# Performance work log

Measured on AMD Instinct MI355X. Metric: run time of the kernel, lower is better.

The kernel has to match this reference:

```python
import jax, jax.numpy as jnp
import numpy as np

KS = 3          # deformable kernel size
N = KS * KS     # 9 sampling points
PAD = 1         # zero padding before sampling


def setup_inputs() -> dict:
    key = jax.random.key(0)
    k = jax.random.split(key, 4)
    b, c, h, w = 8, 64, 128, 128
    x = jax.random.normal(k[0], (b, c, h, w), jnp.float32)
    # offset-prediction conv: Conv2d(c, 2*N, 3, padding=1, stride=1) with bias
    w_off = jax.random.normal(k[1], (2 * N, c, 3, 3), jnp.float32) * 0.01
    b_off = jax.random.normal(k[2], (2 * N,), jnp.float32) * 0.01
    # main conv: Conv2d(c, c, 3, stride=3, bias=None) applied to rearranged samples
    w_conv = jax.random.normal(k[3], (c, c, KS, KS), jnp.float32) * (1.0 / np.sqrt(c * N))
    return {"x": x, "w_off": w_off, "b_off": b_off, "w_conv": w_conv}


def _deform_conv2d(x, w_off, b_off, w_conv):
    b, c, h, w = x.shape
    # 1) predict offsets: (b, 2N, h, w)
    offset = jax.lax.conv_general_dilated(
        x, w_off, (1, 1), ((PAD, PAD), (PAD, PAD)),
        dimension_numbers=("NCHW", "OIHW", "NCHW"))
    offset = offset + b_off[None, :, None, None]
    offset = offset.transpose(0, 2, 3, 1)  # (b, h, w, 2N), first N = rows, last N = cols

    # 2) sampling positions p = p_0 + p_n + offset (in zero-padded coords)
    dx, dy = jnp.meshgrid(
        jnp.arange(-(KS - 1) // 2, (KS - 1) // 2 + 1),
        jnp.arange(-(KS - 1) // 2, (KS - 1) // 2 + 1), indexing="ij")
    pn_x = dx.reshape(-1).astype(x.dtype)  # (N,)
    pn_y = dy.reshape(-1).astype(x.dtype)
    r0 = jnp.arange(1, h + 1, dtype=x.dtype)  # p_0 starts at 1 (padding shift)
    c0 = jnp.arange(1, w + 1, dtype=x.dtype)
    p_x = offset[..., :N] + pn_x + r0[None, :, None, None]   # (b,h,w,N)
    p_y = offset[..., N:] + pn_y + c0[None, None, :, None]

    xp = jnp.pad(x, ((0, 0), (0, 0), (PAD, PAD), (PAD, PAD)))
    Hp, Wp = h + 2 * PAD, w + 2 * PAD

    fx = jnp.floor(p_x)
    fy = jnp.floor(p_y)
    q_lt_x = jnp.clip(fx, 0, Hp - 1).astype(jnp.int32)
    q_lt_y = jnp.clip(fy, 0, Wp - 1).astype(jnp.int32)
    q_rb_x = jnp.clip(fx + 1, 0, Hp - 1).astype(jnp.int32)
    q_rb_y = jnp.clip(fy + 1, 0, Wp - 1).astype(jnp.int32)
    p_x = jnp.clip(p_x, 0, Hp - 1)
    p_y = jnp.clip(p_y, 0, Wp - 1)

    # bilinear weights (b,h,w,N); q values are non-differentiable (int)
    g_lt = (1 + (q_lt_x - p_x)) * (1 + (q_lt_y - p_y))
    g_rb = (1 - (q_rb_x - p_x)) * (1 - (q_rb_y - p_y))
    g_lb = (1 + (q_lt_x - p_x)) * (1 - (q_rb_y - p_y))
    g_rt = (1 - (q_rb_x - p_x)) * (1 + (q_lt_y - p_y))

    xp_flat = xp.reshape(b, c, Hp * Wp)

    def gather(qx, qy):
        idx = (qx * Wp + qy).reshape(b, 1, h * w * N)
        out = jnp.take_along_axis(
            xp_flat, jnp.broadcast_to(idx, (b, c, h * w * N)), axis=2)
        return out.reshape(b, c, h, w, N)

    x_off = (g_lt[:, None] * gather(q_lt_x, q_lt_y)
             + g_rb[:, None] * gather(q_rb_x, q_rb_y)
             + g_lb[:, None] * gather(q_lt_x, q_rb_y)
             + g_rt[:, None] * gather(q_rb_x, q_lt_y))  # (b,c,h,w,N)

    # 3) final KSxKS conv with stride KS over the rearranged samples is exactly
    #    a contraction over the N sampling points (sample n = kernel tap (i,j), n=i*KS+j)
    out = jnp.einsum("bchwn,ocn->bohw", x_off, w_conv.reshape(c, c, N))
    return out


def reference(x, w_off, b_off, w_conv):
    return _deform_conv2d(x, w_off, b_off, w_conv) + x
```

## Files before the change

### kernel.cpp

```cpp
#include <hip/hip_runtime.h>


typedef _Float16 h2    __attribute__((ext_vector_type(2)));
typedef _Float16 f16x8 __attribute__((ext_vector_type(8)));
typedef float    f32x4 __attribute__((ext_vector_type(4)));

#define MFMAH(a, b, c) __builtin_amdgcn_mfma_f32_16x16x32_f16(a, b, c, 0, 0, 0)
#define GTAG 0x40000000
#define OFFS 21

__device__ __forceinline__ h2 bch2(unsigned u) { return __builtin_bit_cast(h2, u); }
__device__ __forceinline__ unsigned bcu(h2 v) { return __builtin_bit_cast(unsigned, v); }
__device__ __forceinline__ unsigned short f2h(float f) {
    return __builtin_bit_cast(unsigned short, (_Float16)f);
}

__global__ __launch_bounds__(256) void k_prep_xt(const float* __restrict__ x,
                                                 unsigned short* __restrict__ xt) {
    __shared__ float xs[64][129];
    const int bh = blockIdx.x;
    const int h = bh & 127, b = bh >> 7;
    const float* xr = x + ((size_t)b * 64 * 128 + h) * 128;
    for (int idx = threadIdx.x; idx < 8192; idx += 256) {
        int c = idx >> 7, w = idx & 127;
        xs[c][w] = xr[(size_t)c * 16384 + w];
    }
    __syncthreads();
    unsigned short* xto = xt + ((size_t)bh << 13);
    for (int j = threadIdx.x; j < 1024; j += 256) {
        int w = j >> 3, c0 = (j & 7) << 3;
        unsigned short tmp[8];
#pragma unroll
        for (int e = 0; e < 8; ++e) tmp[e] = f2h(xs[c0 + e][w]);
        *(uint4*)(xto + w * 64 + c0) = *(const uint4*)tmp;
    }
}

__global__ void k_prep_w(const float* __restrict__ w_conv, const float* __restrict__ w_off,
                         unsigned short* __restrict__ w_m2, unsigned short* __restrict__ woff2) {
    int t = blockIdx.x * 256 + threadIdx.x;
    if (t < 36864) {
        int r = t & 511;
        int fid = t >> 9;
        int l15 = r >> 5, q4 = (r >> 3) & 3, e = t & 7;
        int chunk = fid & 1, of = (fid >> 1) & 3, n = fid >> 3;
        int o = of * 16 + l15, c = chunk * 32 + q4 * 8 + e;
        w_m2[t] = f2h(w_conv[(o * 64 + c) * 9 + n]);
    }
    int t2 = t - 36864;
    if (t2 >= 0 && t2 < 18432) {
        int r = t2 & 511;
        int fid = t2 >> 9;
        int l15 = r >> 5, q4 = (r >> 3) & 3, e = t2 & 7;
        int kc = fid & 1, half = (fid >> 1) & 1, rj = fid >> 2;
        int k = half * 16 + l15, c = kc * 32 + q4 * 8 + e;
        woff2[t2] = (k < 18) ? f2h(w_off[(k * 64 + c) * 9 + rj]) : (unsigned short)0;
    }
}

__global__ __launch_bounds__(256, 2) void k_fused(
    const float* __restrict__ x, const unsigned short* __restrict__ xt,
    const unsigned short* __restrict__ w_m2, const unsigned short* __restrict__ woff2,
    const float* __restrict__ b_off, float* __restrict__ out) {

    __shared__ __align__(16) unsigned char raw[420 * 128];
    __shared__ int   atab[9][64][4];
    __shared__ uint4 gtab[9][64];
    __shared__ float offv[64 * OFFS];
    __shared__ int   sfb;

    const int wk = ((blockIdx.x & 7) << 8) + (blockIdx.x >> 3);
    const int b = wk >> 8, h = (wk >> 1) & 127, wt = (wk & 1) << 6;

    const int tid  = threadIdx.x;
    const int lane = tid & 63, wid = tid >> 6;
    const int l15  = lane & 15, q4 = lane >> 4;
    const int lofs = ((l15 << 2) + q4) << 3;
    const int px   = wid * 16 + l15;

    const unsigned short* xtb = xt + ((size_t)b << 20);

    if (tid == 0) sfb = 0;

    for (int idx = tid; idx < 3360; idx += 256) {
        int rec = idx >> 3, cc = idx & 7;
        int row = rec / 70, col = rec - row * 70;
        int xr = h - 2 + row, xc = wt - 3 + col;
        uint4 v = make_uint4(0, 0, 0, 0);
        if (xr >= 0 && xr < 128 && xc >= 0 && xc < 128)
            v = *(const uint4*)(xtb + ((((size_t)xr << 7) + xc) << 6) + (cc << 3));
        *(uint4*)(raw + (rec << 7) + ((cc ^ (col & 7)) << 4)) = v;
    }
    __syncthreads();

    {
        f32x4 o0 = {0.f, 0.f, 0.f, 0.f}, o1 = {0.f, 0.f, 0.f, 0.f};
#pragma unroll
        for (int rj = 0; rj < 9; ++rj) {
            const int dr = rj / 3, dj = rj % 3;
            const int colw = px + dj + 2;
            const int recb = (dr + 1) * 70 + colw;
            const int swz  = colw & 7;
#pragma unroll
            for (int kc = 0; kc < 2; ++kc) {
                f16x8 bfrag = *(const f16x8*)(raw + (recb << 7) + ((((kc << 2) + q4) ^ swz) << 4));
                f16x8 a0 = *(const f16x8*)((const _Float16*)woff2 + ((((rj * 2 + 0) << 1) + kc) << 9) + lofs);
                f16x8 a1 = *(const f16x8*)((const _Float16*)woff2 + ((((rj * 2 + 1) << 1) + kc) << 9) + lofs);
                o0 = MFMAH(a0, bfrag, o0);
                o1 = MFMAH(a1, bfrag, o1);
            }
        }
#pragma unroll
        for (int rg = 0; rg < 4; ++rg) {
            int o = q4 * 4 + rg;
            offv[px * OFFS + o] = o0[rg] + b_off[o];
            int o1i = 16 + o;
            if (o1i < 18) offv[px * OFFS + o1i] = o1[rg] + b_off[o1i];
        }
    }
    __syncthreads();

    for (int idx = tid; idx < 576; idx += 256) {
        const int n = idx >> 6, p = idx & 63;
        float ox = offv[p * OFFS + n], oy = offv[p * OFFS + 9 + n];
        float pxf = ox + (float)(n / 3 - 1) + (float)(h + 1);
        float pyf = oy + (float)(n % 3 - 1) + (float)(wt + p + 1);
        float fx = floorf(pxf), fy = floorf(pyf);
        float fxc  = fminf(fmaxf(fx, 0.f), 129.f);
        float fyc  = fminf(fmaxf(fy, 0.f), 129.f);
        float fxc1 = fminf(fmaxf(fx + 1.f, 0.f), 129.f);
        float fyc1 = fminf(fmaxf(fy + 1.f, 0.f), 129.f);
        int qltx = (int)fxc, qlty = (int)fyc, qrbx = (int)fxc1, qrby = (int)fyc1;
        pxf = fminf(fmaxf(pxf, 0.f), 129.f);
        pyf = fminf(fmaxf(pyf, 0.f), 129.f);
        float glt = (1.f + (fxc  - pxf)) * (1.f + (fyc  - pyf));
        float grb = (1.f - (fxc1 - pxf)) * (1.f - (fyc1 - pyf));
        float glb = (1.f + (fxc  - pxf)) * (1.f - (fyc1 - pyf));
        float grt = (1.f - (fxc1 - pxf)) * (1.f + (fyc  - pyf));
        bool vlx = (qltx >= 1) & (qltx <= 128), vly = (qlty >= 1) & (qlty <= 128);
        bool vrx = (qrbx >= 1) & (qrbx <= 128), vry = (qrby >= 1) & (qrby <= 128);

        auto enc = [&](int qx, int qy, bool val) -> int {
            if (!val) return 0;
            int wr = qx - h + 1;
            int wc = qy - wt + 2;
            if (wr >= 0 && wr < 6 && wc >= 0 && wc < 70)
                return ((wr * 70 + wc) << 7) | ((wc & 7) << 4);
            return GTAG | ((((qx - 1) << 7) + (qy - 1)) << 6);
        };
        int a0 = enc(qltx, qlty, vlx & vly);
        int a1 = enc(qrbx, qrby, vrx & vry);
        int a2 = enc(qltx, qrby, vlx & vry);
        int a3 = enc(qrbx, qlty, vrx & vly);
        if ((a0 | a1 | a2 | a3) & GTAG) sfb = 1;
        if (!(vlx & vly)) glt = 0.f;
        if (!(vrx & vry)) grb = 0.f;
        if (!(vlx & vry)) glb = 0.f;
        if (!(vrx & vly)) grt = 0.f;
        auto pk = [](float g) -> unsigned {
            _Float16 t = (_Float16)g;
            h2 r = {t, t};
            return __builtin_bit_cast(unsigned, r);
        };
        *(int4*)&atab[n][p][0] = make_int4(a0, a1, a2, a3);
        gtab[n][p] = make_uint4(pk(glt), pk(grb), pk(glb), pk(grt));
    }
    __syncthreads();

    const size_t obase = ((size_t)b * 64 * 128 + h) * 128 + wt + px;
    float xres[4][4];
#pragma unroll
    for (int of = 0; of < 4; ++of)
#pragma unroll
        for (int rg = 0; rg < 4; ++rg)
            xres[of][rg] = x[obase + (size_t)(of * 16 + q4 * 4 + rg) * 16384];

    f32x4 acc[4];
#pragma unroll
    for (int of = 0; of < 4; ++of) acc[of] = (f32x4){0.f, 0.f, 0.f, 0.f};

    const _Float16* wmh = (const _Float16*)w_m2;
    f16x8 wreg[2][2][4];
#pragma unroll
    for (int of = 0; of < 4; ++of) {
        wreg[0][0][of] = *(const f16x8*)(wmh + (((of << 1) + 0) << 9) + lofs);
        wreg[0][1][of] = *(const f16x8*)(wmh + (((of << 1) + 1) << 9) + lofs);
    }

    auto blend = [&](const uint4* clo, const uint4* chi, uint4 gq, f16x8& bfr0, f16x8& bfr1) {
        h2 g0 = bch2(gq.x), g1 = bch2(gq.y), g2 = bch2(gq.z), g3 = bch2(gq.w);
        const unsigned* c0 = (const unsigned*)&clo[0];
        const unsigned* c1 = (const unsigned*)&clo[1];
        const unsigned* c2 = (const unsigned*)&clo[2];
        const unsigned* c3 = (const unsigned*)&clo[3];
        const unsigned* e0 = (const unsigned*)&chi[0];
        const unsigned* e1 = (const unsigned*)&chi[1];
        const unsigned* e2 = (const unsigned*)&chi[2];
        const unsigned* e3 = (const unsigned*)&chi[3];
        unsigned owl[4], owh[4];
#pragma unroll
        for (int d = 0; d < 4; ++d) {
            h2 sl = bch2(c0[d]) * g0;
            sl = __builtin_elementwise_fma(bch2(c1[d]), g1, sl);
            sl = __builtin_elementwise_fma(bch2(c2[d]), g2, sl);
            sl = __builtin_elementwise_fma(bch2(c3[d]), g3, sl);
            owl[d] = bcu(sl);
            h2 sh = bch2(e0[d]) * g0;
            sh = __builtin_elementwise_fma(bch2(e1[d]), g1, sh);
            sh = __builtin_elementwise_fma(bch2(e2[d]), g2, sh);
            sh = __builtin_elementwise_fma(bch2(e3[d]), g3, sh);
            owh[d] = bcu(sh);
        }
        bfr0 = __builtin_bit_cast(f16x8, *(const uint4*)owl);
        bfr1 = __builtin_bit_cast(f16x8, *(const uint4*)owh);
    };

    if (!sfb) {
#pragma unroll
        for (int n = 0; n < 9; ++n) {
            if (n < 8) {
                const _Float16* wn1 = wmh + ((n + 1) << 12);
#pragma unroll
                for (int of = 0; of < 4; ++of) {
                    wreg[(n + 1) & 1][0][of] = *(const f16x8*)(wn1 + (((of << 1) + 0) << 9) + lofs);
                    wreg[(n + 1) & 1][1][of] = *(const f16x8*)(wn1 + (((of << 1) + 1) << 9) + lofs);
                }
            }
            const int4  av = *(const int4*)&atab[n][px][0];
            const uint4 gq = gtab[n][px];
            const int ee[4] = {av.x, av.y, av.z, av.w};
            uint4 clo[4], chi[4];
#pragma unroll
            for (int j = 0; j < 4; ++j) {
                const unsigned char* lp = raw + (ee[j] & ~127);
                int sl = ((q4 ^ (ee[j] >> 4)) & 7) << 4;
                clo[j] = *(const uint4*)(lp + sl);
                chi[j] = *(const uint4*)(lp + (sl ^ 64));
            }
            f16x8 bfr0, bfr1;
            blend(clo, chi, gq, bfr0, bfr1);
#pragma unroll
            for (int of = 0; of < 4; ++of) {
                acc[of] = MFMAH(wreg[n & 1][0][of], bfr0, acc[of]);
                acc[of] = MFMAH(wreg[n & 1][1][of], bfr1, acc[of]);
            }
        }
    } else {
        for (int n = 0; n < 9; ++n) {
            const int4  av = *(const int4*)&atab[n][px][0];
            const uint4 gq = gtab[n][px];
            const int ee[4] = {av.x, av.y, av.z, av.w};
            uint4 clo[4], chi[4];
#pragma unroll
            for (int j = 0; j < 4; ++j) {
                int e = ee[j];
                if (e & GTAG) {
                    const unsigned short* gp = xtb + (e & (GTAG - 1));
                    clo[j] = *(const uint4*)(gp + (q4 << 3));
                    chi[j] = *(const uint4*)(gp + (q4 << 3) + 32);
                } else {
                    const unsigned char* lp = raw + (e & ~127);
                    int sl = ((q4 ^ (e >> 4)) & 7) << 4;
                    clo[j] = *(const uint4*)(lp + sl);
                    chi[j] = *(const uint4*)(lp + (sl ^ 64));
                }
            }
            f16x8 bfr0, bfr1;
            blend(clo, chi, gq, bfr0, bfr1);
            const _Float16* wn = wmh + (n << 12);
#pragma unroll
            for (int of = 0; of < 4; ++of) {
                f16x8 a0 = *(const f16x8*)(wn + (((of << 1) + 0) << 9) + lofs);
                f16x8 a1 = *(const f16x8*)(wn + (((of << 1) + 1) << 9) + lofs);
                acc[of] = MFMAH(a0, bfr0, acc[of]);
                acc[of] = MFMAH(a1, bfr1, acc[of]);
            }
        }
    }

#pragma unroll
    for (int of = 0; of < 4; ++of)
#pragma unroll
        for (int rg = 0; rg < 4; ++rg)
            out[obase + (size_t)(of * 16 + q4 * 4 + rg) * 16384] = acc[of][rg] + xres[of][rg];
}

extern "C" void kernel_launch(void* const* d_in, const int* in_sizes, int n_in,
                              void* d_out, int out_size, void* d_ws, size_t ws_size,
                              hipStream_t stream) {
    const float* x      = (const float*)d_in[0];
    const float* w_off  = (const float*)d_in[1];
    const float* b_off  = (const float*)d_in[2];
    const float* w_conv = (const float*)d_in[3];

    unsigned short* xt    = (unsigned short*)d_ws;
    unsigned short* w_m2  = xt + (size_t)8 * 128 * 128 * 64;
    unsigned short* woff2 = w_m2 + 9 * 64 * 64;

    hipLaunchKernelGGL(k_prep_xt, dim3(1024), dim3(256), 0, stream, x, xt);
    hipLaunchKernelGGL(k_prep_w,  dim3(216),  dim3(256), 0, stream, w_conv, w_off, w_m2, woff2);
    hipLaunchKernelGGL(k_fused,   dim3(2048), dim3(256), 0, stream,
                       x, xt, w_m2, woff2, b_off, (float*)d_out);
}
```

Baseline: 93.24 us.

## Shrink LDS with rolling 4-row ring buffer and inline bilinear setup per tap

The fused kernel now keeps a 4-row ring buffer of the input window in LDS instead of 6 rows, streaming rows 4 and 5 in while taps are processed, with extra barriers. It drops the per-tap address and weight tables and stores offsets as fp16. Bilinear indices and weights are recomputed inline in each tap, and launch bounds are raised to 4 blocks per CU. The goal is higher occupancy from the smaller LDS footprint, at the cost of more ALU work per tap, fp16 offset precision, and the slow path now reading every corner from global memory.

```diff
diff --git a/kernel.cpp b/kernel.cpp
--- a/kernel.cpp
+++ b/kernel.cpp
@@ -6,13 +6,17 @@
 typedef float    f32x4 __attribute__((ext_vector_type(4)));
 
 #define MFMAH(a, b, c) __builtin_amdgcn_mfma_f32_16x16x32_f16(a, b, c, 0, 0, 0)
-#define GTAG 0x40000000
-#define OFFS 21
-
-__device__ __forceinline__ h2 bch2(unsigned u) { return __builtin_bit_cast(h2, u); }
-__device__ __forceinline__ unsigned bcu(h2 v) { return __builtin_bit_cast(unsigned, v); }
+
 __device__ __forceinline__ unsigned short f2h(float f) {
     return __builtin_bit_cast(unsigned short, (_Float16)f);
+}
+__device__ __forceinline__ float h2f_bits(unsigned u) {
+    return (float)__builtin_bit_cast(_Float16, (unsigned short)(u & 0xffffu));
+}
+__device__ __forceinline__ unsigned dup16(float g) {
+    _Float16 t = (_Float16)g;
+    h2 r = {t, t};
+    return __builtin_bit_cast(unsigned, r);
 }
 
 __global__ __launch_bounds__(256) void k_prep_xt(const float* __restrict__ x,
@@ -58,16 +62,14 @@
     }
 }
 
-__global__ __launch_bounds__(256, 2) void k_fused(
+__global__ __launch_bounds__(256, 4) void k_fused(
     const float* __restrict__ x, const unsigned short* __restrict__ xt,
     const unsigned short* __restrict__ w_m2, const unsigned short* __restrict__ woff2,
     const float* __restrict__ b_off, float* __restrict__ out) {
 
-    __shared__ __align__(16) unsigned char raw[420 * 128];
-    __shared__ int   atab[9][64][4];
-    __shared__ uint4 gtab[9][64];
-    __shared__ float offv[64 * OFFS];
-    __shared__ int   sfb;
+    __shared__ __align__(16) unsigned char raw[4 * 70 * 128];
+    __shared__ __align__(16) _Float16 offv[64 * 24];
+    __shared__ int sfb;
 
     const int wk = ((blockIdx.x & 7) << 8) + (blockIdx.x >> 3);
     const int b = wk >> 8, h = (wk >> 1) & 127, wt = (wk & 1) << 6;
@@ -79,13 +81,14 @@
     const int px   = wid * 16 + l15;
 
     const unsigned short* xtb = xt + ((size_t)b << 20);
+    const _Float16* wmh  = (const _Float16*)w_m2;
 
     if (tid == 0) sfb = 0;
 
-    for (int idx = tid; idx < 3360; idx += 256) {
+    for (int idx = tid; idx < 2240; idx += 256) {
         int rec = idx >> 3, cc = idx & 7;
-        int row = rec / 70, col = rec - row * 70;
-        int xr = h - 2 + row, xc = wt - 3 + col;
+        int rl = rec / 70, col = rec - rl * 70;
+        int xr = h - 2 + rl, xc = wt - 3 + col;
         uint4 v = make_uint4(0, 0, 0, 0);
         if (xr >= 0 && xr < 128 && xc >= 0 && xc < 128)
             v = *(const uint4*)(xtb + ((((size_t)xr << 7) + xc) << 6) + (cc << 3));
@@ -110,85 +113,44 @@
                 o1 = MFMAH(a1, bfrag, o1);
             }
         }
+        float4 bo = *(const float4*)(b_off + (q4 << 2));
+        float2 bo2 = *(const float2*)(b_off + 16);
+        const float bov[4] = {bo.x, bo.y, bo.z, bo.w};
 #pragma unroll
         for (int rg = 0; rg < 4; ++rg) {
-            int o = q4 * 4 + rg;
-            offv[px * OFFS + o] = o0[rg] + b_off[o];
-            int o1i = 16 + o;
-            if (o1i < 18) offv[px * OFFS + o1i] = o1[rg] + b_off[o1i];
+            int o = (q4 << 2) + rg;
+            offv[px * 24 + o] = (_Float16)(o0[rg] + bov[rg]);
+            if (q4 == 0 && rg < 2) offv[px * 24 + 16 + rg] = (_Float16)(o1[rg] + (rg ? bo2.y : bo2.x));
         }
     }
     __syncthreads();
 
     for (int idx = tid; idx < 576; idx += 256) {
         const int n = idx >> 6, p = idx & 63;
-        float ox = offv[p * OFFS + n], oy = offv[p * OFFS + 9 + n];
-        float pxf = ox + (float)(n / 3 - 1) + (float)(h + 1);
-        float pyf = oy + (float)(n % 3 - 1) + (float)(wt + p + 1);
+        const int dr = n / 3, dj = n % 3;
+        float ox = (float)offv[p * 24 + n], oy = (float)offv[p * 24 + 9 + n];
+        float pxf = (float)(h + dr) + ox, pyf = (float)(wt + p + dj) + oy;
         float fx = floorf(pxf), fy = floorf(pyf);
-        float fxc  = fminf(fmaxf(fx, 0.f), 129.f);
-        float fyc  = fminf(fmaxf(fy, 0.f), 129.f);
-        float fxc1 = fminf(fmaxf(fx + 1.f, 0.f), 129.f);
-        float fyc1 = fminf(fmaxf(fy + 1.f, 0.f), 129.f);
-        int qltx = (int)fxc, qlty = (int)fyc, qrbx = (int)fxc1, qrby = (int)fyc1;
-        pxf = fminf(fmaxf(pxf, 0.f), 129.f);
-        pyf = fminf(fmaxf(pyf, 0.f), 129.f);
-        float glt = (1.f + (fxc  - pxf)) * (1.f + (fyc  - pyf));
-        float grb = (1.f - (fxc1 - pxf)) * (1.f - (fyc1 - pyf));
-        float glb = (1.f + (fxc  - pxf)) * (1.f - (fyc1 - pyf));
-        float grt = (1.f - (fxc1 - pxf)) * (1.f + (fyc  - pyf));
-        bool vlx = (qltx >= 1) & (qltx <= 128), vly = (qlty >= 1) & (qlty <= 128);
-        bool vrx = (qrbx >= 1) & (qrbx <= 128), vry = (qrby >= 1) & (qrby <= 128);
-
-        auto enc = [&](int qx, int qy, bool val) -> int {
-            if (!val) return 0;
-            int wr = qx - h + 1;
-            int wc = qy - wt + 2;
-            if (wr >= 0 && wr < 6 && wc >= 0 && wc < 70)
-                return ((wr * 70 + wc) << 7) | ((wc & 7) << 4);
-            return GTAG | ((((qx - 1) << 7) + (qy - 1)) << 6);
-        };
-        int a0 = enc(qltx, qlty, vlx & vly);
-        int a1 = enc(qrbx, qrby, vrx & vry);
-        int a2 = enc(qltx, qrby, vlx & vry);
-        int a3 = enc(qrbx, qlty, vrx & vly);
-        if ((a0 | a1 | a2 | a3) & GTAG) sfb = 1;
-        if (!(vlx & vly)) glt = 0.f;
-        if (!(vrx & vry)) grb = 0.f;
-        if (!(vlx & vry)) glb = 0.f;
-        if (!(vrx & vly)) grt = 0.f;
-        auto pk = [](float g) -> unsigned {
-            _Float16 t = (_Float16)g;
-            h2 r = {t, t};
-            return __builtin_bit_cast(unsigned, r);
-        };
-        *(int4*)&atab[n][p][0] = make_int4(a0, a1, a2, a3);
-        gtab[n][p] = make_uint4(pk(glt), pk(grb), pk(glb), pk(grt));
+        int qx0 = (int)fminf(fmaxf(fx, 0.f), 129.f);
+        int qx1 = (int)fminf(fmaxf(fx + 1.f, 0.f), 129.f);
+        int qy0 = (int)fminf(fmaxf(fy, 0.f), 129.f);
+        int qy1 = (int)fminf(fmaxf(fy + 1.f, 0.f), 129.f);
+        int r0 = qx0 - h - dr, r1 = qx1 - h - dr;
+        int c0 = qy0 - wt + 2, c1 = qy1 - wt + 2;
+        bool oow = (r0 < -1) | (r0 > 2) | (r1 < -1) | (r1 > 2) |
+                   (c0 < 0) | (c0 >= 70) | (c1 < 0) | (c1 >= 70);
+        if (oow) sfb = 1;
     }
     __syncthreads();
-
-    const size_t obase = ((size_t)b * 64 * 128 + h) * 128 + wt + px;
-    float xres[4][4];
-#pragma unroll
-    for (int of = 0; of < 4; ++of)
-#pragma unroll
-        for (int rg = 0; rg < 4; ++rg)
-            xres[of][rg] = x[obase + (size_t)(of * 16 + q4 * 4 + rg) * 16384];
+    const bool slow = (sfb != 0);
 
     f32x4 acc[4];
 #pragma unroll
     for (int of = 0; of < 4; ++of) acc[of] = (f32x4){0.f, 0.f, 0.f, 0.f};
 
-    const _Float16* wmh = (const _Float16*)w_m2;
-    f16x8 wreg[2][2][4];
-#pragma unroll
-    for (int of = 0; of < 4; ++of) {
-        wreg[0][0][of] = *(const f16x8*)(wmh + (((of << 1) + 0) << 9) + lofs);
-        wreg[0][1][of] = *(const f16x8*)(wmh + (((of << 1) + 1) << 9) + lofs);
-    }
-
     auto blend = [&](const uint4* clo, const uint4* chi, uint4 gq, f16x8& bfr0, f16x8& bfr1) {
-        h2 g0 = bch2(gq.x), g1 = bch2(gq.y), g2 = bch2(gq.z), g3 = bch2(gq.w);
+        h2 g0 = __builtin_bit_cast(h2, gq.x), g1 = __builtin_bit_cast(h2, gq.y);
+        h2 g2 = __builtin_bit_cast(h2, gq.z), g3 = __builtin_bit_cast(h2, gq.w);
         const unsigned* c0 = (const unsigned*)&clo[0];
         const unsigned* c1 = (const unsigned*)&clo[1];
         const unsigned* c2 = (const unsigned*)&clo[2];
@@ -200,71 +162,153 @@
         unsigned owl[4], owh[4];
 #pragma unroll
         for (int d = 0; d < 4; ++d) {
-            h2 sl = bch2(c0[d]) * g0;
-            sl = __builtin_elementwise_fma(bch2(c1[d]), g1, sl);
-            sl = __builtin_elementwise_fma(bch2(c2[d]), g2, sl);
-            sl = __builtin_elementwise_fma(bch2(c3[d]), g3, sl);
-            owl[d] = bcu(sl);
-            h2 sh = bch2(e0[d]) * g0;
-            sh = __builtin_elementwise_fma(bch2(e1[d]), g1, sh);
-            sh = __builtin_elementwise_fma(bch2(e2[d]), g2, sh);
-            sh = __builtin_elementwise_fma(bch2(e3[d]), g3, sh);
-            owh[d] = bcu(sh);
+            h2 sl = __builtin_bit_cast(h2, c0[d]) * g0;
+            sl = __builtin_elementwise_fma(__builtin_bit_cast(h2, c1[d]), g1, sl);
+            sl = __builtin_elementwise_fma(__builtin_bit_cast(h2, c2[d]), g2, sl);
+            sl = __builtin_elementwise_fma(__builtin_bit_cast(h2, c3[d]), g3, sl);
+            owl[d] = __builtin_bit_cast(unsigned, sl);
+            h2 sh = __builtin_bit_cast(h2, e0[d]) * g0;
+            sh = __builtin_elementwise_fma(__builtin_bit_cast(h2, e1[d]), g1, sh);
+            sh = __builtin_elementwise_fma(__builtin_bit_cast(h2, e2[d]), g2, sh);
+            sh = __builtin_elementwise_fma(__builtin_bit_cast(h2, e3[d]), g3, sh);
+            owh[d] = __builtin_bit_cast(unsigned, sh);
         }
         bfr0 = __builtin_bit_cast(f16x8, *(const uint4*)owl);
         bfr1 = __builtin_bit_cast(f16x8, *(const uint4*)owh);
     };
 
-    if (!sfb) {
-#pragma unroll
+    if (!slow) {
+        const unsigned* op = (const unsigned*)(offv + px * 24);
+        uint4 oA = *(const uint4*)op;
+        uint4 oB = *(const uint4*)(op + 4);
+        unsigned oC = op[8];
+        const unsigned ow[9] = {oA.x, oA.y, oA.z, oA.w, oB.x, oB.y, oB.z, oB.w, oC};
+#define OX(n) h2f_bits(ow[(n) >> 1] >> (((n) & 1) << 4))
+#define OY(n) h2f_bits(ow[(9 + (n)) >> 1] >> (((9 + (n)) & 1) << 4))
+
+        uint4 pf[3];
+        int pcol[3], pcc[3];
+#pragma unroll
+        for (int k = 0; k < 3; ++k) {
+            int idx = tid + (k << 8);
+            bool v = idx < 560;
+            int rec = idx >> 3;
+            pcol[k] = v ? rec : 0;
+            pcc[k]  = idx & 7;
+            int xr = h + 2, xc = wt - 3 + pcol[k];
+            uint4 vv = make_uint4(0, 0, 0, 0);
+            if (v && xr < 128 && xc >= 0 && xc < 128)
+                vv = *(const uint4*)(xtb + ((((size_t)xr << 7) + xc) << 6) + (pcc[k] << 3));
+            if (!v) pcol[k] = -1;
+            pf[k] = vv;
+        }
+
+#define TAP(n)                                                                           \
+        {                                                                                \
+            constexpr int dr = (n) / 3, dj = (n) % 3;                                    \
+            const _Float16* wn = wmh + ((n) << 12);                                      \
+            f16x8 wa0[4], wa1[4];                                                        \
+            _Pragma("unroll")                                                            \
+            for (int of = 0; of < 4; ++of) {                                             \
+                wa0[of] = *(const f16x8*)(wn + (((of << 1) + 0) << 9) + lofs);           \
+                wa1[of] = *(const f16x8*)(wn + (((of << 1) + 1) << 9) + lofs);           \
+            }                                                                            \
+            float ox = OX(n), oy = OY(n);                                                \
+            float pxf = (float)(h + dr) + ox, pyf = (float)(wt + px + dj) + oy;          \
+            float fx = floorf(pxf), fy = floorf(pyf);                                    \
+            float qx0f = fminf(fmaxf(fx, 0.f), 129.f);                                   \
+            float qx1f = fminf(fmaxf(fx + 1.f, 0.f), 129.f);                             \
+            float qy0f = fminf(fmaxf(fy, 0.f), 129.f);                                   \
+            float qy1f = fminf(fmaxf(fy + 1.f, 0.f), 129.f);                             \
+            float pxc = fminf(fmaxf(pxf, 0.f), 129.f);                                   \
+            float pyc = fminf(fmaxf(pyf, 0.f), 129.f);                                   \
+            float ax0 = 1.f + (qx0f - pxc), ax1 = 1.f - (qx1f - pxc);                    \
+            float ay0 = 1.f + (qy0f - pyc), ay1 = 1.f - (qy1f - pyc);                    \
+            int s0 = ((((int)qx0f + 1 - h) & 3) * 70) << 7;                              \
+            int s1 = ((((int)qx1f + 1 - h) & 3) * 70) << 7;                              \
+            int c0 = (int)qy0f - wt + 2, c1 = (int)qy1f - wt + 2;                        \
+            int blt = s0 + (c0 << 7), brb = s1 + (c1 << 7);                              \
+            int blb = s0 + (c1 << 7), brt = s1 + (c0 << 7);                              \
+            int z0 = ((q4 ^ c0) & 7) << 4, z1 = ((q4 ^ c1) & 7) << 4;                    \
+            uint4 clo[4], chi[4];                                                        \
+            clo[0] = *(const uint4*)(raw + blt + z0); chi[0] = *(const uint4*)(raw + blt + (z0 ^ 64)); \
+            clo[1] = *(const uint4*)(raw + brb + z1); chi[1] = *(const uint4*)(raw + brb + (z1 ^ 64)); \
+            clo[2] = *(const uint4*)(raw + blb + z1); chi[2] = *(const uint4*)(raw + blb + (z1 ^ 64)); \
+            clo[3] = *(const uint4*)(raw + brt + z0); chi[3] = *(const uint4*)(raw + brt + (z0 ^ 64)); \
+            uint4 gq = make_uint4(dup16(ax0 * ay0), dup16(ax1 * ay1),                    \
+                                  dup16(ax0 * ay1), dup16(ax1 * ay0));                   \
+            f16x8 bfr0, bfr1;                                                            \
+            blend(clo, chi, gq, bfr0, bfr1);                                             \
+            _Pragma("unroll")                                                            \
+            for (int of = 0; of < 4; ++of) {                                             \
+                acc[of] = MFMAH(wa0[of], bfr0, acc[of]);                                 \
+                acc[of] = MFMAH(wa1[of], bfr1, acc[of]);                                 \
+            }                                                                            \
+        }
+
+        TAP(0) TAP(1) TAP(2)
+        __syncthreads();
+#pragma unroll
+        for (int k = 0; k < 3; ++k)
+            if (pcol[k] >= 0)
+                *(uint4*)(raw + ((0 * 70 + pcol[k]) << 7) + ((pcc[k] ^ (pcol[k] & 7)) << 4)) = pf[k];
+        __syncthreads();
+#pragma unroll
+        for (int k = 0; k < 3; ++k) {
+            int idx = tid + (k << 8);
+            bool v = idx < 560;
+            int rec = idx >> 3;
+            pcol[k] = v ? rec : -1;
+            pcc[k]  = idx & 7;
+            int xr = h + 3, xc = wt - 3 + rec;
+            uint4 vv = make_uint4(0, 0, 0, 0);
+            if (v && xr < 128 && xc >= 0 && xc < 128)
+                vv = *(const uint4*)(xtb + ((((size_t)xr << 7) + xc) << 6) + (pcc[k] << 3));
+            pf[k] = vv;
+        }
+        TAP(3) TAP(4) TAP(5)
+        __syncthreads();
+#pragma unroll
+        for (int k = 0; k < 3; ++k)
+            if (pcol[k] >= 0)
+                *(uint4*)(raw + ((1 * 70 + pcol[k]) << 7) + ((pcc[k] ^ (pcol[k] & 7)) << 4)) = pf[k];
+        __syncthreads();
+        TAP(6) TAP(7) TAP(8)
+#undef TAP
+#undef OX
+#undef OY
+    } else {
         for (int n = 0; n < 9; ++n) {
-            if (n < 8) {
-                const _Float16* wn1 = wmh + ((n + 1) << 12);
-#pragma unroll
-                for (int of = 0; of < 4; ++of) {
-                    wreg[(n + 1) & 1][0][of] = *(const f16x8*)(wn1 + (((of << 1) + 0) << 9) + lofs);
-                    wreg[(n + 1) & 1][1][of] = *(const f16x8*)(wn1 + (((of << 1) + 1) << 9) + lofs);
+            const int dr = n / 3, dj = n % 3;
+            float ox = (float)offv[px * 24 + n], oy = (float)offv[px * 24 + 9 + n];
+            float pxf = (float)(h + dr) + ox, pyf = (float)(wt + px + dj) + oy;
+            float fx = floorf(pxf), fy = floorf(pyf);
+            float qx0f = fminf(fmaxf(fx, 0.f), 129.f);
+            float qx1f = fminf(fmaxf(fx + 1.f, 0.f), 129.f);
+            float qy0f = fminf(fmaxf(fy, 0.f), 129.f);
+            float qy1f = fminf(fmaxf(fy + 1.f, 0.f), 129.f);
+            float pxc = fminf(fmaxf(pxf, 0.f), 129.f);
+            float pyc = fminf(fmaxf(pyf, 0.f), 129.f);
+            float ax0 = 1.f + (qx0f - pxc), ax1 = 1.f - (qx1f - pxc);
+            float ay0 = 1.f + (qy0f - pyc), ay1 = 1.f - (qy1f - pyc);
+            int qx[2] = {(int)qx0f, (int)qx1f};
+            int qy[2] = {(int)qy0f, (int)qy1f};
+            uint4 clo[4], chi[4];
+            const int rsel[4] = {0, 1, 0, 1}, csel[4] = {0, 1, 1, 0};
+#pragma unroll
+            for (int j = 0; j < 4; ++j) {
+                int rx = qx[rsel[j]], ry = qy[csel[j]];
+                bool v = (rx >= 1) & (rx <= 128) & (ry >= 1) & (ry <= 128);
+                clo[j] = make_uint4(0, 0, 0, 0);
+                chi[j] = make_uint4(0, 0, 0, 0);
+                if (v) {
+                    const unsigned short* gp = xtb + ((((size_t)(rx - 1) << 7) + (ry - 1)) << 6);
+                    clo[j] = *(const uint4*)(gp + (q4 << 3));
+                    chi[j] = *(const uint4*)(gp + (q4 << 3) + 32);
                 }
             }
-            const int4  av = *(const int4*)&atab[n][px][0];
-            const uint4 gq = gtab[n][px];
-            const int ee[4] = {av.x, av.y, av.z, av.w};
-            uint4 clo[4], chi[4];
-#pragma unroll
-            for (int j = 0; j < 4; ++j) {
-                const unsigned char* lp = raw + (ee[j] & ~127);
-                int sl = ((q4 ^ (ee[j] >> 4)) & 7) << 4;
-                clo[j] = *(const uint4*)(lp + sl);
-                chi[j] = *(const uint4*)(lp + (sl ^ 64));
-            }
-            f16x8 bfr0, bfr1;
-            blend(clo, chi, gq, bfr0, bfr1);
-#pragma unroll
-            for (int of = 0; of < 4; ++of) {
-                acc[of] = MFMAH(wreg[n & 1][0][of], bfr0, acc[of]);
-                acc[of] = MFMAH(wreg[n & 1][1][of], bfr1, acc[of]);
-            }
-        }
-    } else {
-        for (int n = 0; n < 9; ++n) {
-            const int4  av = *(const int4*)&atab[n][px][0];
-            const uint4 gq = gtab[n][px];
-            const int ee[4] = {av.x, av.y, av.z, av.w};
-            uint4 clo[4], chi[4];
-#pragma unroll
-            for (int j = 0; j < 4; ++j) {
-                int e = ee[j];
-                if (e & GTAG) {
-                    const unsigned short* gp = xtb + (e & (GTAG - 1));
-                    clo[j] = *(const uint4*)(gp + (q4 << 3));
-                    chi[j] = *(const uint4*)(gp + (q4 << 3) + 32);
-                } else {
-                    const unsigned char* lp = raw + (e & ~127);
-                    int sl = ((q4 ^ (e >> 4)) & 7) << 4;
-                    clo[j] = *(const uint4*)(lp + sl);
-                    chi[j] = *(const uint4*)(lp + (sl ^ 64));
-                }
-            }
+            uint4 gq = make_uint4(dup16(ax0 * ay0), dup16(ax1 * ay1),
+                                  dup16(ax0 * ay1), dup16(ax1 * ay0));
             f16x8 bfr0, bfr1;
             blend(clo, chi, gq, bfr0, bfr1);
             const _Float16* wn = wmh + (n << 12);
@@ -278,11 +322,14 @@
         }
     }
 
+    const size_t obase = ((size_t)b * 64 * 128 + h) * 128 + wt + px;
 #pragma unroll
     for (int of = 0; of < 4; ++of)
 #pragma unroll
-        for (int rg = 0; rg < 4; ++rg)
-            out[obase + (size_t)(of * 16 + q4 * 4 + rg) * 16384] = acc[of][rg] + xres[of][rg];
+        for (int rg = 0; rg < 4; ++rg) {
+            size_t a = obase + (size_t)((of << 4) + (q4 << 2) + rg) * 16384;
+            out[a] = acc[of][rg] + x[a];
+        }
 }
 
 extern "C" void kernel_launch(void* const* d_in, const int* in_sizes, int n_in,
```

Result: faster. 84.55 us (-9.3%).
